# Performance work log

Hardware: AMD Instinct MI355X
Metric: run time of the kernel (lower is better)

Reference implementation:

```python
import jax, jax.numpy as jnp
import numpy as np

N_LEVELS, CPL = 4, 1024           # levels, cells per level (n_cells = 4096)
IN_D, HID, OUT_D, MLP = 512, 1024, 512, 128


def setup_inputs() -> dict:
    key = jax.random.key(0)
    ks = iter(jax.random.split(key, 32))
    r = lambda shape, s=0.05: jax.random.normal(next(ks), shape, dtype=jnp.float32) * s
    inp = {
        'x': r((1, IN_D), 1.0),
        'hiddens': r((N_LEVELS * CPL, HID), 0.1),
        'ea_W1': r((N_LEVELS, IN_D + HID, MLP)), 'ea_b1': r((N_LEVELS, MLP)),
        'ea_W2': r((N_LEVELS, MLP, OUT_D)),      'ea_b2': r((N_LEVELS, OUT_D)),
        'eg_W1': r((N_LEVELS, IN_D + HID, MLP)), 'eg_b1': r((N_LEVELS, MLP)),
        'eg_W2': r((N_LEVELS, MLP, OUT_D)),      'eg_b2': r((N_LEVELS, OUT_D)),
        'gru_Wih': r((N_LEVELS, 3 * HID, OUT_D + 1)),
        'gru_Whh': r((N_LEVELS, 3 * HID, HID)),
        'gru_bih': r((N_LEVELS, 3 * HID)), 'gru_bhh': r((N_LEVELS, 3 * HID)),
        'pred_W1': r((N_LEVELS - 1, HID, HID)), 'pred_b1': r((N_LEVELS - 1, HID)),
        'pred_W2': r((N_LEVELS - 1, HID, HID)), 'pred_b2': r((N_LEVELS - 1, HID)),
        'pei_W': r((HID * N_LEVELS, OUT_D)), 'pei_b': r((OUT_D,)),
        'step': 10,
    }
    return inp


def _forward(x, hiddens, ea_W1, ea_b1, ea_W2, ea_b2, eg_W1, eg_b1, eg_W2, eg_b2,
             gru_Wih, gru_Whh, gru_bih, gru_bhh, pred_W1, pred_b1, pred_W2, pred_b2,
             pei_W, pei_b, step):
    L = gru_Whh.shape[0]
    Hd = gru_Whh.shape[2]
    C = hiddens.shape[0] // L
    h = hiddens.reshape(L, C, Hd)                              # [L,C,H]
    xb = jnp.broadcast_to(x[0], (L, C, x.shape[-1]))           # same x for every cell
    comb = jnp.concatenate([xb, h], axis=-1)                   # [L,C,IN+H]

    def mlp(W1, b1, W2, b2):
        z = jax.nn.relu(jnp.einsum('lci,lim->lcm', comb, W1) + b1[:, None, :])
        return jnp.einsum('lcm,lmo->lco', z, W2) + b2[:, None, :]

    out = mlp(ea_W1, ea_b1, ea_W2, ea_b2) - mlp(eg_W1, eg_b1, eg_W2, eg_b2)  # a - g
    tension = jnp.mean(out ** 2, axis=-1, keepdims=True)       # [L,C,1]
    avg_tension = jnp.mean(tension)                            # mean over all cells

    # GRUCell (torch gate order r,z,n); mem input is detached in the original
    mem_in = jax.lax.stop_gradient(jnp.concatenate([out, tension], axis=-1))  # [L,C,OUT+1]
    gi = jnp.einsum('lci,lgi->lcg', mem_in, gru_Wih) + gru_bih[:, None, :]
    gh = jnp.einsum('lch,lgh->lcg', h, gru_Whh) + gru_bhh[:, None, :]
    i_r, i_z, i_n = jnp.split(gi, 3, axis=-1)
    h_r, h_z, h_n = jnp.split(gh, 3, axis=-1)
    rg = jax.nn.sigmoid(i_r + h_r)
    zg = jax.nn.sigmoid(i_z + h_z)
    ng = jnp.tanh(i_n + rg * h_n)
    new_h = jax.lax.stop_gradient((1.0 - zg) * ng + zg * h)    # self.hiddens = ...detach()

    level_means = new_h.mean(axis=1)                           # [L,H] (pre pe-update)

    # top-down predictors: predicted[lv] from level_means[lv+1]
    pz = jax.nn.relu(jnp.einsum('li,lim->lm', level_means[1:], pred_W1) + pred_b1)
    predicted = jnp.einsum('lm,lmo->lo', pz, pred_W2) + pred_b2          # [L-1,H]
    pe_signal = jax.lax.stop_gradient((predicted - level_means[:-1]) * 0.05)
    delta = jnp.zeros_like(level_means).at[:-1].add(pe_signal).at[1:].add(-0.5 * pe_signal)
    hh = new_h + delta[:, None, :]

    # per-level mean blend
    hh = 0.85 * hh + 0.15 * hh.mean(axis=1, keepdims=True)
    # faction sync: with n_factions == n_levels, factions == levels exactly
    hh = 0.85 * hh + 0.15 * hh.mean(axis=1, keepdims=True)
    if step > 5:  # debate (step is a static Python int)
        global_op = hh.mean(axis=1).mean(axis=0)               # [H]
        dc = max(1, C // 4)
        hh = hh.at[:, :dc].set(0.85 * hh[:, :dc] + 0.15 * global_op)

    combined = level_means.reshape(-1) @ pei_W + pei_b         # [OUT]
    return combined, avg_tension, hh.reshape(-1, Hd)


def reference(x, hiddens, ea_W1, ea_b1, ea_W2, ea_b2, eg_W1, eg_b1, eg_W2, eg_b2,
              gru_Wih, gru_Whh, gru_bih, gru_bhh, pred_W1, pred_b1, pred_W2, pred_b2,
              pei_W, pei_b, step):
    return _forward(x, hiddens, ea_W1, ea_b1, ea_W2, ea_b2, eg_W1, eg_b1, eg_W2, eg_b2,
                    gru_Wih, gru_Whh, gru_bih, gru_bhh, pred_W1, pred_b1, pred_W2, pred_b2,
                    pei_W, pei_b, step)
```

## Files before the change

### kernel.cpp

```cpp
#include <hip/hip_runtime.h>
#include <math.h>

#define L4   4
#define CPL  1024
#define HID  1024
#define IND  512
#define MLPD 128
#define OUTD 512
#define G3   3072
#define ROWS 4096
#define KP   544
#define SCL  0.0009765625f

typedef unsigned short u16;
typedef u16   u16x8  __attribute__((ext_vector_type(8)));
typedef short bf16x8 __attribute__((ext_vector_type(8)));
typedef float f32x4  __attribute__((ext_vector_type(4)));

__device__ __forceinline__ float b2f(u16 u) {
  return __uint_as_float(((unsigned int)u) << 16);
}
__device__ __forceinline__ u16 f2b(float f) {
  unsigned int x = __float_as_uint(f);
  x += 0x7fffu + ((x >> 16) & 1u);
  return (u16)(x >> 16);
}
__device__ __forceinline__ float sigm(float v) { return 1.0f/(1.0f + expf(-v)); }

__device__ __forceinline__ float ld1(const void* p, size_t i, bool f32) {
  return f32 ? ((const float*)p)[i] : b2f(((const u16*)p)[i]);
}
__device__ __forceinline__ void st1(void* p, size_t i, float v, bool f32) {
  if (f32) ((float*)p)[i] = v; else ((u16*)p)[i] = f2b(v);
}
__device__ __forceinline__ u16x8 ldc8(const void* p, size_t i, bool f32) {
  u16x8 r;
  if (f32) {
    const float* q = (const float*)p + i;
    float4 v0 = *reinterpret_cast<const float4*>(q);
    float4 v1 = *reinterpret_cast<const float4*>(q + 4);
    r[0]=f2b(v0.x); r[1]=f2b(v0.y); r[2]=f2b(v0.z); r[3]=f2b(v0.w);
    r[4]=f2b(v1.x); r[5]=f2b(v1.y); r[6]=f2b(v1.z); r[7]=f2b(v1.w);
  } else {
    r = *reinterpret_cast<const u16x8*>((const u16*)p + i);
  }
  return r;
}

__global__ void k_detect(const void* __restrict__ x, int* __restrict__ flag) {
  int t = threadIdx.x;
  const u16* xu = (const u16*)x;
  unsigned u = xu[2*t];
  int e = (u >> 7) & 0xFF;
  int good = (e >= 96 && e <= 134) ? 1 : 0;
  __shared__ int cnt[256];
  cnt[t] = good;
  __syncthreads();
  for (int s = 128; s > 0; s >>= 1) { if (t < s) cnt[t] += cnt[t+s]; __syncthreads(); }
  if (t == 0) flag[0] = (cnt[0] < 200) ? 1 : 0;
}

__global__ void k_prep(float* __restrict__ zf, const void* __restrict__ bih,
                       const void* __restrict__ bhh, const int* __restrict__ dflag,
                       float* __restrict__ bs_r, float* __restrict__ bs_z,
                       float* __restrict__ bn_i, float* __restrict__ bn_h) {
  const bool f32 = dflag[0] != 0;
  int b = blockIdx.x, t = threadIdx.x;
  if (b < 16) {
    int idx = b*256 + t;
    int l = idx >> 10, j = idx & 1023;
    bs_r[idx] = ld1(bih, l*G3 + j, f32)        + ld1(bhh, l*G3 + j, f32);
    bs_z[idx] = ld1(bih, l*G3 + 1024 + j, f32) + ld1(bhh, l*G3 + 1024 + j, f32);
    bn_i[idx] = ld1(bih, l*G3 + 2048 + j, f32);
    bn_h[idx] = ld1(bhh, l*G3 + 2048 + j, f32);
  } else {
    int idx = (b-16)*256 + t;
    zf[idx] = 0.0f;
  }
}

__global__ void k_prep_wih(const void* __restrict__ Wih, const int* __restrict__ dflag,
                           u16* __restrict__ WihP) {
  const bool f32 = dflag[0] != 0;
  int row = blockIdx.x;
  int t = threadIdx.x;
  size_t src = (size_t)row * 513;
  size_t dst = (size_t)row * KP;
  WihP[dst + t]       = f2b(ld1(Wih, src + t, f32));
  WihP[dst + 256 + t] = f2b(ld1(Wih, src + 256 + t, f32));
  if (t < 32) {
    float v = (t == 0) ? ld1(Wih, src + 512, f32) : 0.0f;
    WihP[dst + 512 + t] = f2b(v);
  }
}

__global__ void k_prep_cvt(const void* __restrict__ Whh, const void* __restrict__ H,
                           const int* __restrict__ dflag,
                           u16* __restrict__ WhhP, u16* __restrict__ HB) {
  const bool f32 = dflag[0] != 0;
  int t = threadIdx.x;
  int b = blockIdx.x;
  int c8 = (t & 127) * 8;
  if (b < 6144) {
    int row = b*2 + (t >> 7);
    size_t off = (size_t)row * HID + c8;
    *reinterpret_cast<u16x8*>(&WhhP[off]) = ldc8(Whh, off, f32);
  } else {
    int row = (b - 6144)*2 + (t >> 7);
    size_t off = (size_t)row * HID + c8;
    *reinterpret_cast<u16x8*>(&HB[off]) = ldc8(H, off, f32);
  }
}

__global__ void k_prep_w1t(const void* __restrict__ eaW1, const void* __restrict__ egW1,
                           const int* __restrict__ dflag, u16* __restrict__ W1T) {
  const bool f32 = dflag[0] != 0;
  __shared__ u16 sT[128*66];
  int l = blockIdx.x, path = blockIdx.y, kt = blockIdx.z;
  int t = threadIdx.x;
  const void* W1 = path ? egW1 : eaW1;
  for (int rr = 0; rr < 64; rr += 2) {
    int r = rr + (t >> 7), m = t & 127;
    float v = ld1(W1, ((size_t)l*1536 + 512 + kt*64 + r)*MLPD + m, f32);
    sT[m*66 + r] = f2b(v);
  }
  __syncthreads();
  for (int mm = 0; mm < 128; mm += 4) {
    int m = mm + (t >> 6), kk = t & 63;
    W1T[((size_t)l*256 + path*128 + m)*1024 + kt*64 + kk] = sT[m*66 + kk];
  }
}

__global__ void k_prep_w2m(const void* __restrict__ eaW2, const void* __restrict__ egW2,
                           const int* __restrict__ dflag, u16* __restrict__ W2M) {
  const bool f32 = dflag[0] != 0;
  __shared__ u16 sT[128*130];
  int l = blockIdx.x, path = blockIdx.y, ot = blockIdx.z;
  int t = threadIdx.x;
  const void* W2 = path ? egW2 : eaW2;
  float sgn = path ? -1.0f : 1.0f;
  for (int rr = 0; rr < 128; rr += 2) {
    int r = rr + (t >> 7), o = t & 127;
    float v = ld1(W2, ((size_t)l*MLPD + r)*OUTD + ot*128 + o, f32);
    sT[o*130 + r] = f2b(sgn*v);
  }
  __syncthreads();
  for (int oo = 0; oo < 128; oo += 2) {
    int o = oo + (t >> 7), m = t & 127;
    W2M[((size_t)l*OUTD + ot*128 + o)*256 + path*128 + m] = sT[o*130 + m];
  }
}

__global__ void k_base_acc(const void* __restrict__ x, const void* __restrict__ eaW1,
                           const void* __restrict__ egW1, const int* __restrict__ dflag,
                           float* __restrict__ baseacc) {
  const bool f32 = dflag[0] != 0;
  int l = blockIdx.x, path = blockIdx.y, kc = blockIdx.z, m = threadIdx.x;
  const void* W1 = path ? egW1 : eaW1;
  float acc = 0.0f;
  int i0 = kc*128;
  for (int i = i0; i < i0 + 128; ++i)
    acc += ld1(x, i, f32) * ld1(W1, ((size_t)l*1536 + i)*MLPD + m, f32);
  atomicAdd(&baseacc[path*512 + l*MLPD + m], acc);
}

#define SWZ(row, ku) ((row)*64 + ((ku) ^ (((row)&7)<<3)))

__global__ __launch_bounds__(256) void k_z_mfma(
    const u16* __restrict__ HB, const u16* __restrict__ W1T,
    const void* __restrict__ eab1, const void* __restrict__ egb1,
    const float* __restrict__ baseacc, const int* __restrict__ dflag,
    u16* __restrict__ Z) {
  const bool f32 = dflag[0] != 0;
  __shared__ __align__(16) u16 sA[2][64*64];
  __shared__ __align__(16) u16 sB[2][64*64];
  int t = threadIdx.x;
  int row0 = blockIdx.x * 64;
  int n0   = blockIdx.y * 64;
  int l    = row0 >> 10;
  int wid = t >> 6, lane = t & 63;
  int waveM = wid >> 1, waveN = wid & 1;
  int quad = lane >> 4, lcol = lane & 15;

  f32x4 acc[2][2];
  const f32x4 zz = {0.0f,0.0f,0.0f,0.0f};
#pragma unroll
  for (int i = 0; i < 2; ++i)
#pragma unroll
    for (int j = 0; j < 2; ++j) acc[i][j] = zz;

  u16x8 ra[2], rb[2];
  auto loadk = [&](int k0) {
#pragma unroll
    for (int s = 0; s < 2; ++s) {
      int idx = s*256 + t, row = idx >> 3, ch = idx & 7;
      ra[s] = *reinterpret_cast<const u16x8*>(
          HB + (size_t)(row0 + row)*HID + k0 + ch*8);
      rb[s] = *reinterpret_cast<const u16x8*>(
          W1T + ((size_t)l*256 + n0 + row)*1024 + k0 + ch*8);
    }
  };
  auto stage = [&](int cb) {
#pragma unroll
    for (int s = 0; s < 2; ++s) {
      int idx = s*256 + t, row = idx >> 3, ch = idx & 7;
      *reinterpret_cast<u16x8*>(&sA[cb][SWZ(row, ch*8)]) = ra[s];
      *reinterpret_cast<u16x8*>(&sB[cb][SWZ(row, ch*8)]) = rb[s];
    }
  };

  int cur = 0;
  loadk(0);
  for (int k0 = 0; k0 < HID; k0 += 64) {
    stage(cur);
    asm volatile("s_waitcnt lgkmcnt(0)" ::: "memory");
    __builtin_amdgcn_s_barrier();
    if (k0 + 64 < HID) loadk(k0 + 64);
    __builtin_amdgcn_s_setprio(1);
#pragma unroll
    for (int kc = 0; kc < 2; ++kc) {
      bf16x8 af[2];
#pragma unroll
      for (int i = 0; i < 2; ++i) {
        int rl = waveM*32 + i*16 + lcol;
        af[i] = *reinterpret_cast<const bf16x8*>(&sA[cur][SWZ(rl, kc*32 + quad*8)]);
      }
#pragma unroll
      for (int j = 0; j < 2; ++j) {
        int jl = waveN*32 + j*16 + lcol;
        bf16x8 bf = *reinterpret_cast<const bf16x8*>(&sB[cur][SWZ(jl, kc*32 + quad*8)]);
#pragma unroll
        for (int i = 0; i < 2; ++i)
          acc[i][j] = __builtin_amdgcn_mfma_f32_16x16x32_bf16(af[i], bf, acc[i][j], 0, 0, 0);
      }
    }
    __builtin_amdgcn_s_setprio(0);
    cur ^= 1;
  }
#pragma unroll
  for (int j = 0; j < 2; ++j) {
    int nn = n0 + waveN*32 + j*16 + lcol;
    int path = nn >> 7, m = nn & 127;
    float bval = baseacc[path*512 + l*MLPD + m] +
                 ld1(path ? egb1 : eab1, l*MLPD + m, f32);
#pragma unroll
    for (int i = 0; i < 2; ++i)
#pragma unroll
      for (int g = 0; g < 4; ++g) {
        int r = row0 + waveM*32 + i*16 + quad*4 + g;
        float v = acc[i][j][g] + bval;
        Z[(size_t)r*256 + nn] = f2b(v > 0.0f ? v : 0.0f);
      }
  }
}

__global__ __launch_bounds__(256) void k_outm(
    const u16* __restrict__ Zb, const u16* __restrict__ W2M,
    const void* __restrict__ eab2, const void* __restrict__ egb2,
    const int* __restrict__ dflag, u16* __restrict__ OUTT) {
  const bool f32 = dflag[0] != 0;
  __shared__ __align__(16) u16 sA[2][128*64];
  __shared__ __align__(16) u16 sB[2][64*64];
  int t = threadIdx.x;
  int row0 = blockIdx.x * 128;
  int n0   = blockIdx.y * 64;
  int l    = row0 >> 10;
  int wid = t >> 6, lane = t & 63;
  int waveM = wid & 1, waveJ = wid >> 1;
  int quad = lane >> 4, lcol = lane & 15;

  f32x4 acc[4][2];
  const f32x4 zz = {0.0f,0.0f,0.0f,0.0f};
#pragma unroll
  for (int i = 0; i < 4; ++i)
#pragma unroll
    for (int j = 0; j < 2; ++j) acc[i][j] = zz;

  u16x8 ra[4], rb[2];
  auto loadk = [&](int k0) {
#pragma unroll
    for (int s = 0; s < 4; ++s) {
      int idx = s*256 + t, row = idx >> 3, ch = idx & 7;
      ra[s] = *reinterpret_cast<const u16x8*>(
          Zb + (size_t)(row0 + row)*256 + k0 + ch*8);
    }
#pragma unroll
    for (int s = 0; s < 2; ++s) {
      int idx = s*256 + t, row = idx >> 3, ch = idx & 7;
      rb[s] = *reinterpret_cast<const u16x8*>(
          W2M + ((size_t)l*OUTD + n0 + row)*256 + k0 + ch*8);
    }
  };
  auto stage = [&](int cb) {
#pragma unroll
    for (int s = 0; s < 4; ++s) {
      int idx = s*256 + t, row = idx >> 3, ch = idx & 7;
      *reinterpret_cast<u16x8*>(&sA[cb][SWZ(row, ch*8)]) = ra[s];
    }
#pragma unroll
    for (int s = 0; s < 2; ++s) {
      int idx = s*256 + t, row = idx >> 3, ch = idx & 7;
      *reinterpret_cast<u16x8*>(&sB[cb][SWZ(row, ch*8)]) = rb[s];
    }
  };

  int cur = 0;
  loadk(0);
  for (int k0 = 0; k0 < 256; k0 += 64) {
    stage(cur);
    asm volatile("s_waitcnt lgkmcnt(0)" ::: "memory");
    __builtin_amdgcn_s_barrier();
    if (k0 + 64 < 256) loadk(k0 + 64);
    __builtin_amdgcn_s_setprio(1);
#pragma unroll
    for (int kc = 0; kc < 2; ++kc) {
      bf16x8 af[4];
#pragma unroll
      for (int i = 0; i < 4; ++i) {
        int rl = waveM*64 + i*16 + lcol;
        af[i] = *reinterpret_cast<const bf16x8*>(&sA[cur][SWZ(rl, kc*32 + quad*8)]);
      }
#pragma unroll
      for (int jj = 0; jj < 2; ++jj) {
        int jl = waveJ*32 + jj*16 + lcol;
        bf16x8 bf = *reinterpret_cast<const bf16x8*>(&sB[cur][SWZ(jl, kc*32 + quad*8)]);
#pragma unroll
        for (int i = 0; i < 4; ++i)
          acc[i][jj] = __builtin_amdgcn_mfma_f32_16x16x32_bf16(af[i], bf, acc[i][jj], 0, 0, 0);
      }
    }
    __builtin_amdgcn_s_setprio(0);
    cur ^= 1;
  }
#pragma unroll
  for (int jj = 0; jj < 2; ++jj) {
    int o = n0 + waveJ*32 + jj*16 + lcol;
    float bd = ld1(eab2, l*OUTD + o, f32) - ld1(egb2, l*OUTD + o, f32);
#pragma unroll
    for (int i = 0; i < 4; ++i)
#pragma unroll
      for (int g = 0; g < 4; ++g) {
        int r = row0 + waveM*64 + i*16 + quad*4 + g;
        OUTT[(size_t)r*KP + o] = f2b(acc[i][jj][g] + bd);
      }
  }
}

__global__ void k_tension(u16* __restrict__ OUTT, float* __restrict__ tsum) {
  int row = blockIdx.x, t = threadIdx.x;
  u16* p = OUTT + (size_t)row*KP;
  float v0 = b2f(p[t]), v1 = b2f(p[t+256]);
  float s = v0*v0 + v1*v1;
#pragma unroll
  for (int off = 32; off > 0; off >>= 1) s += __shfl_down(s, off, 64);
  __shared__ float red[4];
  if ((t & 63) == 0) red[t >> 6] = s;
  __syncthreads();
  if (t == 0) {
    float tot = red[0] + red[1] + red[2] + red[3];
    p[512] = f2b(tot * (1.0f/512.0f));
    atomicAdd(tsum, tot);
  }
  if (t < 31) p[513 + t] = 0;
}

__global__ __launch_bounds__(256, 2) void k_gru_mfma(
    const u16* __restrict__ OUTT, const u16* __restrict__ HB,
    const u16* __restrict__ WihP, const u16* __restrict__ WhhP,
    const void* __restrict__ H,
    const float* __restrict__ bs_r, const float* __restrict__ bs_z,
    const float* __restrict__ bn_i, const float* __restrict__ bn_h,
    const int* __restrict__ dflag, void* __restrict__ outv) {
  const bool f32 = dflag[0] != 0;
  __shared__ __align__(16) u16 sA[2][128*64];
  __shared__ __align__(16) u16 sB[2][3*64*64];
  int t = threadIdx.x;
  int bid = blockIdx.x;
  int xg = bid & 7, inner = bid >> 3;
  int l = xg & 3, jG = xg >> 2;
  int rbi = inner & 7, jbl = inner >> 3;
  int row0 = (l*8 + rbi) * 128;
  int j0   = (jG*8 + jbl) * 64;
  int wid = t >> 6, lane = t & 63;
  int waveM = wid & 1, waveJ = wid >> 1;
  int quad = lane >> 4, lcol = lane & 15;

  f32x4 acc[4][4][2];
  const f32x4 zz = {0.0f,0.0f,0.0f,0.0f};
#pragma unroll
  for (int b = 0; b < 4; ++b)
#pragma unroll
    for (int i = 0; i < 4; ++i)
#pragma unroll
      for (int j = 0; j < 2; ++j) acc[b][i][j] = zz;

  u16x8 ra[4], rbr[6];
  auto load1 = [&](int k0) {
    int kw = KP - k0;
#pragma unroll
    for (int s = 0; s < 4; ++s) {
      int idx = s*256 + t, row = idx >> 3, ch = idx & 7;
      if (ch*8 < kw)
        ra[s] = *reinterpret_cast<const u16x8*>(
            OUTT + (size_t)(row0 + row)*KP + k0 + ch*8);
      else { u16x8 z = {0,0,0,0,0,0,0,0}; ra[s] = z; }
    }
#pragma unroll
    for (int s = 0; s < 6; ++s) {
      int idx = s*256 + t, band = idx >> 9, rem = idx & 511;
      int row = rem >> 3, ch = rem & 7;
      if (ch*8 < kw)
        rbr[s] = *reinterpret_cast<const u16x8*>(
            WihP + ((size_t)l*G3 + band*1024 + j0 + row)*KP + k0 + ch*8);
      else { u16x8 z = {0,0,0,0,0,0,0,0}; rbr[s] = z; }
    }
  };
  auto load2 = [&](int k0) {
#pragma unroll
    for (int s = 0; s < 4; ++s) {
      int idx = s*256 + t, row = idx >> 3, ch = idx & 7;
      ra[s] = *reinterpret_cast<const u16x8*>(
          HB + (size_t)(row0 + row)*HID + k0 + ch*8);
    }
#pragma unroll
    for (int s = 0; s < 6; ++s) {
      int idx = s*256 + t, band = idx >> 9, rem = idx & 511;
      int row = rem >> 3, ch = rem & 7;
      rbr[s] = *reinterpret_cast<const u16x8*>(
          WhhP + ((size_t)l*G3 + band*1024 + j0 + row)*HID + k0 + ch*8);
    }
  };
  auto stage = [&](int cb) {
#pragma unroll
    for (int s = 0; s < 4; ++s) {
      int idx = s*256 + t, row = idx >> 3, ch = idx & 7;
      *reinterpret_cast<u16x8*>(&sA[cb][SWZ(row, ch*8)]) = ra[s];
    }
#pragma unroll
    for (int s = 0; s < 6; ++s) {
      int idx = s*256 + t, band = idx >> 9, rem = idx & 511;
      int row = rem >> 3, ch = rem & 7;
      *reinterpret_cast<u16x8*>(&sB[cb][band*4096 + SWZ(row, ch*8)]) = rbr[s];
    }
  };

  int cur = 0;
  load1(0);
  for (int k0 = 0; k0 < KP; k0 += 64) {
    stage(cur);
    asm volatile("s_waitcnt lgkmcnt(0)" ::: "memory");
    __builtin_amdgcn_s_barrier();
    if (k0 + 64 < KP) load1(k0 + 64);
    else              load2(0);
    __builtin_amdgcn_s_setprio(1);
#pragma unroll
    for (int kc = 0; kc < 2; ++kc) {
      bf16x8 af[4];
#pragma unroll
      for (int i = 0; i < 4; ++i) {
        int rl = waveM*64 + i*16 + lcol;
        af[i] = *reinterpret_cast<const bf16x8*>(&sA[cur][SWZ(rl, kc*32 + quad*8)]);
      }
#pragma unroll
      for (int b = 0; b < 3; ++b)
#pragma unroll
        for (int jj = 0; jj < 2; ++jj) {
          int jl = waveJ*32 + jj*16 + lcol;
          bf16x8 bf = *reinterpret_cast<const bf16x8*>(
              &sB[cur][b*4096 + SWZ(jl, kc*32 + quad*8)]);
#pragma unroll
          for (int i = 0; i < 4; ++i)
            acc[b][i][jj] = __builtin_amdgcn_mfma_f32_16x16x32_bf16(
                af[i], bf, acc[b][i][jj], 0, 0, 0);
        }
    }
    __builtin_amdgcn_s_setprio(0);
    cur ^= 1;
  }
  for (int k0 = 0; k0 < HID; k0 += 64) {
    stage(cur);
    asm volatile("s_waitcnt lgkmcnt(0)" ::: "memory");
    __builtin_amdgcn_s_barrier();
    if (k0 + 64 < HID) load2(k0 + 64);
    __builtin_amdgcn_s_setprio(1);
#pragma unroll
    for (int kc = 0; kc < 2; ++kc) {
      bf16x8 af[4];
#pragma unroll
      for (int i = 0; i < 4; ++i) {
        int rl = waveM*64 + i*16 + lcol;
        af[i] = *reinterpret_cast<const bf16x8*>(&sA[cur][SWZ(rl, kc*32 + quad*8)]);
      }
#pragma unroll
      for (int b = 0; b < 3; ++b) {
        int ai = (b < 2) ? b : 3;
#pragma unroll
        for (int jj = 0; jj < 2; ++jj) {
          int jl = waveJ*32 + jj*16 + lcol;
          bf16x8 bf = *reinterpret_cast<const bf16x8*>(
              &sB[cur][b*4096 + SWZ(jl, kc*32 + quad*8)]);
#pragma unroll
          for (int i = 0; i < 4; ++i)
            acc[ai][i][jj] = __builtin_amdgcn_mfma_f32_16x16x32_bf16(
                af[i], bf, acc[ai][i][jj], 0, 0, 0);
        }
      }
    }
    __builtin_amdgcn_s_setprio(0);
    cur ^= 1;
  }
#pragma unroll
  for (int i = 0; i < 4; ++i)
#pragma unroll
    for (int jj = 0; jj < 2; ++jj) {
      int j = j0 + waveJ*32 + jj*16 + lcol;
      float br = bs_r[l*HID + j], bz = bs_z[l*HID + j];
      float bi = bn_i[l*HID + j], bh = bn_h[l*HID + j];
#pragma unroll
      for (int g = 0; g < 4; ++g) {
        int r = row0 + waveM*64 + i*16 + quad*4 + g;
        float rg = sigm(acc[0][i][jj][g] + br);
        float zg = sigm(acc[1][i][jj][g] + bz);
        float ng = tanhf(acc[2][i][jj][g] + bi + rg*(acc[3][i][jj][g] + bh));
        float hv = ld1(H, (size_t)r*HID + j, f32);
        st1(outv, 513 + (size_t)r*HID + j, (1.0f - zg)*ng + zg*hv, f32);
      }
    }
}

__global__ void k_lm_acc(const void* __restrict__ outv, const int* __restrict__ dflag,
                         float* __restrict__ lm) {
  const bool f32 = dflag[0] != 0;
  int l = blockIdx.x, cc = blockIdx.y, t = threadIdx.x;
  float s0=0.f, s1=0.f, s2=0.f, s3=0.f;
  for (int c = cc*16; c < cc*16 + 16; ++c) {
    size_t base = 513 + (size_t)(l*CPL + c)*HID;
    s0 += ld1(outv, base + t,       f32);
    s1 += ld1(outv, base + 256 + t, f32);
    s2 += ld1(outv, base + 512 + t, f32);
    s3 += ld1(outv, base + 768 + t, f32);
  }
  atomicAdd(&lm[l*HID + t],       s0);
  atomicAdd(&lm[l*HID + 256 + t], s1);
  atomicAdd(&lm[l*HID + 512 + t], s2);
  atomicAdd(&lm[l*HID + 768 + t], s3);
}

__global__ void k_pz_acc(const float* __restrict__ lm, const void* __restrict__ pW1,
                         const int* __restrict__ dflag, float* __restrict__ pz) {
  const bool f32 = dflag[0] != 0;
  int lv = blockIdx.x, mb = blockIdx.y, kc = blockIdx.z;
  int m = mb*256 + threadIdx.x;
  float acc = 0.0f;
  int i0 = kc*32;
  const float* lmp = lm + (lv + 1)*HID;
  for (int i = i0; i < i0 + 32; ++i)
    acc += lmp[i] * ld1(pW1, ((size_t)lv*HID + i)*HID + m, f32);
  atomicAdd(&pz[lv*HID + m], acc * SCL);
}
__global__ void k_pzfin(float* __restrict__ pz, const void* __restrict__ pb1,
                        const int* __restrict__ dflag) {
  const bool f32 = dflag[0] != 0;
  int idx = blockIdx.x*256 + threadIdx.x;
  float v = pz[idx] + ld1(pb1, idx, f32);
  pz[idx] = v > 0.0f ? v : 0.0f;
}
__global__ void k_pe_acc(const float* __restrict__ pz, const void* __restrict__ pW2,
                         const int* __restrict__ dflag, float* __restrict__ pe) {
  const bool f32 = dflag[0] != 0;
  int lv = blockIdx.x, ob = blockIdx.y, kc = blockIdx.z;
  int o = ob*256 + threadIdx.x;
  float acc = 0.0f;
  int m0 = kc*32;
  const float* pzp = pz + lv*HID;
  for (int m = m0; m < m0 + 32; ++m)
    acc += pzp[m] * ld1(pW2, ((size_t)lv*HID + m)*HID + o, f32);
  atomicAdd(&pe[lv*HID + o], acc);
}
__global__ void k_pefin(float* __restrict__ pe, const void* __restrict__ pb2,
                        const float* __restrict__ lm, const int* __restrict__ dflag) {
  const bool f32 = dflag[0] != 0;
  int idx = blockIdx.x*256 + threadIdx.x;
  pe[idx] = (pe[idx] + ld1(pb2, idx, f32) - lm[idx]*SCL) * 0.05f;
}

__global__ void k_addc_gop(const float* __restrict__ lm, const float* __restrict__ pe,
                           float* __restrict__ addc, float* __restrict__ gop) {
  int j = blockIdx.x*256 + threadIdx.x;
  float pe0 = pe[j], pe1 = pe[1024 + j], pe2 = pe[2048 + j];
  float d0 = pe0, d1 = pe1 - 0.5f*pe0, d2 = pe2 - 0.5f*pe1, d3 = -0.5f*pe2;
  float l0 = lm[j]*SCL, l1 = lm[1024 + j]*SCL, l2 = lm[2048 + j]*SCL, l3 = lm[3072 + j]*SCL;
  addc[j]        = 0.2775f*l0 + d0;
  addc[1024 + j] = 0.2775f*l1 + d1;
  addc[2048 + j] = 0.2775f*l2 + d2;
  addc[3072 + j] = 0.2775f*l3 + d3;
  gop[j] = 0.25f*((l0 + d0) + (l1 + d1) + (l2 + d2) + (l3 + d3));
}

__global__ void k_comb_acc(const float* __restrict__ lm, const void* __restrict__ peiW,
                           const int* __restrict__ dflag, float* __restrict__ comb) {
  const bool f32 = dflag[0] != 0;
  int ob = blockIdx.x, kc = blockIdx.y;
  int o = ob*256 + threadIdx.x;
  float acc = 0.0f;
  int i0 = kc*128;
  for (int i = i0; i < i0 + 128; ++i)
    acc += lm[i] * ld1(peiW, (size_t)i*OUTD + o, f32);
  atomicAdd(&comb[o], acc * SCL);
}
__global__ void k_fin(const float* __restrict__ comb, const void* __restrict__ peib,
                      const float* __restrict__ tsum, const int* __restrict__ dflag,
                      void* __restrict__ outv) {
  const bool f32 = dflag[0] != 0;
  int o = blockIdx.x*256 + threadIdx.x;
  st1(outv, o, comb[o] + ld1(peib, o, f32), f32);
  if (o == 0) st1(outv, 512, tsum[0] * (1.0f/(4096.0f*512.0f)), f32);
}

__global__ void k_hh(void* __restrict__ outv, const float* __restrict__ addc,
                     const float* __restrict__ gop, const int* __restrict__ step,
                     const int* __restrict__ dflag) {
  const bool f32 = dflag[0] != 0;
  int row = blockIdx.x, t = threadIdx.x;
  int l = row >> 10, c = row & 1023;
  bool debate = (step[0] > 5) && (c < 256);
  size_t base = 513 + (size_t)row*HID;
#pragma unroll
  for (int k = 0; k < 4; ++k) {
    int j = t + k*256;
    float v = 0.7225f * ld1(outv, base + j, f32) + addc[l*HID + j];
    if (debate) v = 0.85f*v + 0.15f*gop[j];
    st1(outv, base + j, v, f32);
  }
}

extern "C" void kernel_launch(void* const* d_in, const int* in_sizes, int n_in,
                              void* d_out, int out_size, void* d_ws, size_t ws_size,
                              hipStream_t stream) {
  (void)in_sizes; (void)n_in; (void)out_size; (void)ws_size;
  const void* x    = d_in[0];
  const void* hid  = d_in[1];
  const void* eaW1 = d_in[2];
  const void* eab1 = d_in[3];
  const void* eaW2 = d_in[4];
  const void* eab2 = d_in[5];
  const void* egW1 = d_in[6];
  const void* egb1 = d_in[7];
  const void* egW2 = d_in[8];
  const void* egb2 = d_in[9];
  const void* gWih = d_in[10];
  const void* gWhh = d_in[11];
  const void* gbih = d_in[12];
  const void* gbhh = d_in[13];
  const void* pW1  = d_in[14];
  const void* pb1  = d_in[15];
  const void* pW2  = d_in[16];
  const void* pb2  = d_in[17];
  const void* peiW = d_in[18];
  const void* peib = d_in[19];
  const int*  step = (const int*)d_in[20];

  float* wsf = (float*)d_ws;
  float* tsum    = wsf + 0;
  float* baseacc = wsf + 64;
  float* lm      = wsf + 1088;
  float* pz      = wsf + 5184;
  float* pe      = wsf + 8256;
  float* comb    = wsf + 11328;
  int*   dflag   = (int*)(wsf + 12288);
  float* bs_r    = wsf + 12352;
  float* bs_z    = wsf + 16448;
  float* bn_i    = wsf + 20544;
  float* bn_h    = wsf + 24640;
  float* addc    = wsf + 28736;
  float* gop     = wsf + 32832;
  u16* Zb   = (u16*)(wsf + 33856);
  u16* OUTT = Zb + (size_t)4096*256;
  u16* WihP = OUTT + (size_t)4096*KP;
  u16* HB   = WihP + (size_t)12288*KP;
  u16* WhhP = HB   + (size_t)4096*1024;
  u16* W2M  = WhhP + (size_t)12288*1024;
  u16* W1T  = OUTT;

  k_detect   <<<dim3(1),        dim3(256), 0, stream>>>(x, dflag);
  k_prep     <<<dim3(64),       dim3(256), 0, stream>>>(wsf, gbih, gbhh, dflag,
                                                        bs_r, bs_z, bn_i, bn_h);
  k_prep_wih <<<dim3(12288),    dim3(256), 0, stream>>>(gWih, dflag, WihP);
  k_prep_cvt <<<dim3(8192),     dim3(256), 0, stream>>>(gWhh, hid, dflag, WhhP, HB);
  k_prep_w1t <<<dim3(4,2,16),   dim3(256), 0, stream>>>(eaW1, egW1, dflag, W1T);
  k_prep_w2m <<<dim3(4,2,4),    dim3(256), 0, stream>>>(eaW2, egW2, dflag, W2M);
  k_base_acc <<<dim3(4,2,4),    dim3(128), 0, stream>>>(x, eaW1, egW1, dflag, baseacc);
  k_z_mfma   <<<dim3(64,4),     dim3(256), 0, stream>>>(HB, W1T, eab1, egb1,
                                                        baseacc, dflag, Zb);
  k_outm     <<<dim3(32,8),     dim3(256), 0, stream>>>(Zb, W2M, eab2, egb2,
                                                        dflag, OUTT);
  k_tension  <<<dim3(4096),     dim3(256), 0, stream>>>(OUTT, tsum);
  k_gru_mfma <<<dim3(512),      dim3(256), 0, stream>>>(OUTT, HB, WihP, WhhP, hid,
                                                        bs_r, bs_z, bn_i, bn_h,
                                                        dflag, d_out);
  k_lm_acc   <<<dim3(4,64),     dim3(256), 0, stream>>>(d_out, dflag, lm);
  k_pz_acc   <<<dim3(3,4,32),   dim3(256), 0, stream>>>(lm, pW1, dflag, pz);
  k_pzfin    <<<dim3(12),       dim3(256), 0, stream>>>(pz, pb1, dflag);
  k_pe_acc   <<<dim3(3,4,32),   dim3(256), 0, stream>>>(pz, pW2, dflag, pe);
  k_pefin    <<<dim3(12),       dim3(256), 0, stream>>>(pe, pb2, lm, dflag);
  k_addc_gop <<<dim3(4),        dim3(256), 0, stream>>>(lm, pe, addc, gop);
  k_comb_acc <<<dim3(2,32),     dim3(256), 0, stream>>>(lm, peiW, dflag, comb);
  k_fin      <<<dim3(2),        dim3(256), 0, stream>>>(comb, peib, tsum, dflag, d_out);
  k_hh       <<<dim3(4096),     dim3(256), 0, stream>>>(d_out, addc, gop, step, dflag);
}
```

Measured before the change: 477.7 us.

## Deepen GRU MFMA global prefetch to two stages and fuse small epilogue kernels

```diff
diff --git a/kernel.cpp b/kernel.cpp
--- a/kernel.cpp
+++ b/kernel.cpp
@@ -394,64 +394,60 @@
 #pragma unroll
       for (int j = 0; j < 2; ++j) acc[b][i][j] = zz;
 
-  u16x8 ra[4], rbr[6];
-  auto load1 = [&](int k0) {
-    int kw = KP - k0;
-#pragma unroll
-    for (int s = 0; s < 4; ++s) {
-      int idx = s*256 + t, row = idx >> 3, ch = idx & 7;
-      if (ch*8 < kw)
-        ra[s] = *reinterpret_cast<const u16x8*>(
-            OUTT + (size_t)(row0 + row)*KP + k0 + ch*8);
-      else { u16x8 z = {0,0,0,0,0,0,0,0}; ra[s] = z; }
-    }
-#pragma unroll
-    for (int s = 0; s < 6; ++s) {
-      int idx = s*256 + t, band = idx >> 9, rem = idx & 511;
+  u16x8 raA[4], rbA[6], raB[4], rbB[6];
+
+  auto loadS = [&](u16x8 (&ra)[4], u16x8 (&rb)[6], int s) {
+    if (s < 9) {
+      int k0 = s*64;
+      int kw = KP - k0;
+#pragma unroll
+      for (int q = 0; q < 4; ++q) {
+        int idx = q*256 + t, row = idx >> 3, ch = idx & 7;
+        if (ch*8 < kw)
+          ra[q] = *reinterpret_cast<const u16x8*>(
+              OUTT + (size_t)(row0 + row)*KP + k0 + ch*8);
+        else { u16x8 z = {0,0,0,0,0,0,0,0}; ra[q] = z; }
+      }
+#pragma unroll
+      for (int q = 0; q < 6; ++q) {
+        int idx = q*256 + t, band = idx >> 9, rem = idx & 511;
+        int row = rem >> 3, ch = rem & 7;
+        if (ch*8 < kw)
+          rb[q] = *reinterpret_cast<const u16x8*>(
+              WihP + ((size_t)l*G3 + band*1024 + j0 + row)*KP + k0 + ch*8);
+        else { u16x8 z = {0,0,0,0,0,0,0,0}; rb[q] = z; }
+      }
+    } else {
+      int k0 = (s - 9)*64;
+#pragma unroll
+      for (int q = 0; q < 4; ++q) {
+        int idx = q*256 + t, row = idx >> 3, ch = idx & 7;
+        ra[q] = *reinterpret_cast<const u16x8*>(
+            HB + (size_t)(row0 + row)*HID + k0 + ch*8);
+      }
+#pragma unroll
+      for (int q = 0; q < 6; ++q) {
+        int idx = q*256 + t, band = idx >> 9, rem = idx & 511;
+        int row = rem >> 3, ch = rem & 7;
+        rb[q] = *reinterpret_cast<const u16x8*>(
+            WhhP + ((size_t)l*G3 + band*1024 + j0 + row)*HID + k0 + ch*8);
+      }
+    }
+  };
+  auto stage = [&](int cb, u16x8 (&ra)[4], u16x8 (&rb)[6]) {
+#pragma unroll
+    for (int q = 0; q < 4; ++q) {
+      int idx = q*256 + t, row = idx >> 3, ch = idx & 7;
+      *reinterpret_cast<u16x8*>(&sA[cb][SWZ(row, ch*8)]) = ra[q];
+    }
+#pragma unroll
+    for (int q = 0; q < 6; ++q) {
+      int idx = q*256 + t, band = idx >> 9, rem = idx & 511;
       int row = rem >> 3, ch = rem & 7;
-      if (ch*8 < kw)
-        rbr[s] = *reinterpret_cast<const u16x8*>(
-            WihP + ((size_t)l*G3 + band*1024 + j0 + row)*KP + k0 + ch*8);
-      else { u16x8 z = {0,0,0,0,0,0,0,0}; rbr[s] = z; }
+      *reinterpret_cast<u16x8*>(&sB[cb][band*4096 + SWZ(row, ch*8)]) = rb[q];
     }
   };
-  auto load2 = [&](int k0) {
-#pragma unroll
-    for (int s = 0; s < 4; ++s) {
-      int idx = s*256 + t, row = idx >> 3, ch = idx & 7;
-      ra[s] = *reinterpret_cast<const u16x8*>(
-          HB + (size_t)(row0 + row)*HID + k0 + ch*8);
-    }
-#pragma unroll
-    for (int s = 0; s < 6; ++s) {
-      int idx = s*256 + t, band = idx >> 9, rem = idx & 511;
-      int row = rem >> 3, ch = rem & 7;
-      rbr[s] = *reinterpret_cast<const u16x8*>(
-          WhhP + ((size_t)l*G3 + band*1024 + j0 + row)*HID + k0 + ch*8);
-    }
-  };
-  auto stage = [&](int cb) {
-#pragma unroll
-    for (int s = 0; s < 4; ++s) {
-      int idx = s*256 + t, row = idx >> 3, ch = idx & 7;
-      *reinterpret_cast<u16x8*>(&sA[cb][SWZ(row, ch*8)]) = ra[s];
-    }
-#pragma unroll
-    for (int s = 0; s < 6; ++s) {
-      int idx = s*256 + t, band = idx >> 9, rem = idx & 511;
-      int row = rem >> 3, ch = rem & 7;
-      *reinterpret_cast<u16x8*>(&sB[cb][band*4096 + SWZ(row, ch*8)]) = rbr[s];
-    }
-  };
-
-  int cur = 0;
-  load1(0);
-  for (int k0 = 0; k0 < KP; k0 += 64) {
-    stage(cur);
-    asm volatile("s_waitcnt lgkmcnt(0)" ::: "memory");
-    __builtin_amdgcn_s_barrier();
-    if (k0 + 64 < KP) load1(k0 + 64);
-    else              load2(0);
+  auto domfma = [&](int cb, bool g2) {
     __builtin_amdgcn_s_setprio(1);
 #pragma unroll
     for (int kc = 0; kc < 2; ++kc) {
@@ -459,46 +455,16 @@
 #pragma unroll
       for (int i = 0; i < 4; ++i) {
         int rl = waveM*64 + i*16 + lcol;
-        af[i] = *reinterpret_cast<const bf16x8*>(&sA[cur][SWZ(rl, kc*32 + quad*8)]);
-      }
-#pragma unroll
-      for (int b = 0; b < 3; ++b)
+        af[i] = *reinterpret_cast<const bf16x8*>(&sA[cb][SWZ(rl, kc*32 + quad*8)]);
+      }
+#pragma unroll
+      for (int b = 0; b < 3; ++b) {
+        int ai = (g2 && b == 2) ? 3 : b;
 #pragma unroll
         for (int jj = 0; jj < 2; ++jj) {
           int jl = waveJ*32 + jj*16 + lcol;
           bf16x8 bf = *reinterpret_cast<const bf16x8*>(
-              &sB[cur][b*4096 + SWZ(jl, kc*32 + quad*8)]);
-#pragma unroll
-          for (int i = 0; i < 4; ++i)
-            acc[b][i][jj] = __builtin_amdgcn_mfma_f32_16x16x32_bf16(
-                af[i], bf, acc[b][i][jj], 0, 0, 0);
-        }
-    }
-    __builtin_amdgcn_s_setprio(0);
-    cur ^= 1;
-  }
-  for (int k0 = 0; k0 < HID; k0 += 64) {
-    stage(cur);
-    asm volatile("s_waitcnt lgkmcnt(0)" ::: "memory");
-    __builtin_amdgcn_s_barrier();
-    if (k0 + 64 < HID) load2(k0 + 64);
-    __builtin_amdgcn_s_setprio(1);
-#pragma unroll
-    for (int kc = 0; kc < 2; ++kc) {
-      bf16x8 af[4];
-#pragma unroll
-      for (int i = 0; i < 4; ++i) {
-        int rl = waveM*64 + i*16 + lcol;
-        af[i] = *reinterpret_cast<const bf16x8*>(&sA[cur][SWZ(rl, kc*32 + quad*8)]);
-      }
-#pragma unroll
-      for (int b = 0; b < 3; ++b) {
-        int ai = (b < 2) ? b : 3;
-#pragma unroll
-        for (int jj = 0; jj < 2; ++jj) {
-          int jl = waveJ*32 + jj*16 + lcol;
-          bf16x8 bf = *reinterpret_cast<const bf16x8*>(
-              &sB[cur][b*4096 + SWZ(jl, kc*32 + quad*8)]);
+              &sB[cb][b*4096 + SWZ(jl, kc*32 + quad*8)]);
 #pragma unroll
           for (int i = 0; i < 4; ++i)
             acc[ai][i][jj] = __builtin_amdgcn_mfma_f32_16x16x32_bf16(
@@ -507,7 +473,27 @@
       }
     }
     __builtin_amdgcn_s_setprio(0);
+  };
+
+  const int NS = 25;
+  int cur = 0;
+  loadS(raA, rbA, 0);
+  loadS(raB, rbB, 1);
+  for (int s = 0; s < NS; s += 2) {
+    stage(cur, raA, rbA);
+    asm volatile("s_waitcnt lgkmcnt(0)" ::: "memory");
+    __builtin_amdgcn_s_barrier();
+    if (s + 2 < NS) loadS(raA, rbA, s + 2);
+    domfma(cur, s >= 9);
     cur ^= 1;
+    if (s + 1 < NS) {
+      stage(cur, raB, rbB);
+      asm volatile("s_waitcnt lgkmcnt(0)" ::: "memory");
+      __builtin_amdgcn_s_barrier();
+      if (s + 3 < NS) loadS(raB, rbB, s + 3);
+      domfma(cur, s + 1 >= 9);
+      cur ^= 1;
+    }
   }
 #pragma unroll
   for (int i = 0; i < 4; ++i)
@@ -558,36 +544,30 @@
     acc += lmp[i] * ld1(pW1, ((size_t)lv*HID + i)*HID + m, f32);
   atomicAdd(&pz[lv*HID + m], acc * SCL);
 }
-__global__ void k_pzfin(float* __restrict__ pz, const void* __restrict__ pb1,
-                        const int* __restrict__ dflag) {
-  const bool f32 = dflag[0] != 0;
-  int idx = blockIdx.x*256 + threadIdx.x;
-  float v = pz[idx] + ld1(pb1, idx, f32);
-  pz[idx] = v > 0.0f ? v : 0.0f;
-}
-__global__ void k_pe_acc(const float* __restrict__ pz, const void* __restrict__ pW2,
+__global__ void k_pe_acc(const float* __restrict__ pz, const void* __restrict__ pb1,
+                         const void* __restrict__ pW2,
                          const int* __restrict__ dflag, float* __restrict__ pe) {
   const bool f32 = dflag[0] != 0;
   int lv = blockIdx.x, ob = blockIdx.y, kc = blockIdx.z;
   int o = ob*256 + threadIdx.x;
   float acc = 0.0f;
   int m0 = kc*32;
-  const float* pzp = pz + lv*HID;
-  for (int m = m0; m < m0 + 32; ++m)
-    acc += pzp[m] * ld1(pW2, ((size_t)lv*HID + m)*HID + o, f32);
+  for (int m = m0; m < m0 + 32; ++m) {
+    float v = pz[lv*HID + m] + ld1(pb1, lv*HID + m, f32);
+    v = v > 0.0f ? v : 0.0f;
+    acc += v * ld1(pW2, ((size_t)lv*HID + m)*HID + o, f32);
+  }
   atomicAdd(&pe[lv*HID + o], acc);
 }
-__global__ void k_pefin(float* __restrict__ pe, const void* __restrict__ pb2,
-                        const float* __restrict__ lm, const int* __restrict__ dflag) {
-  const bool f32 = dflag[0] != 0;
-  int idx = blockIdx.x*256 + threadIdx.x;
-  pe[idx] = (pe[idx] + ld1(pb2, idx, f32) - lm[idx]*SCL) * 0.05f;
-}
 
 __global__ void k_addc_gop(const float* __restrict__ lm, const float* __restrict__ pe,
+                           const void* __restrict__ pb2, const int* __restrict__ dflag,
                            float* __restrict__ addc, float* __restrict__ gop) {
+  const bool f32 = dflag[0] != 0;
   int j = blockIdx.x*256 + threadIdx.x;
-  float pe0 = pe[j], pe1 = pe[1024 + j], pe2 = pe[2048 + j];
+  float pe0 = (pe[j]        + ld1(pb2, j,        f32) - lm[j]*SCL)        * 0.05f;
+  float pe1 = (pe[1024 + j] + ld1(pb2, 1024 + j, f32) - lm[1024 + j]*SCL) * 0.05f;
+  float pe2 = (pe[2048 + j] + ld1(pb2, 2048 + j, f32) - lm[2048 + j]*SCL) * 0.05f;
   float d0 = pe0, d1 = pe1 - 0.5f*pe0, d2 = pe2 - 0.5f*pe1, d3 = -0.5f*pe2;
   float l0 = lm[j]*SCL, l1 = lm[1024 + j]*SCL, l2 = lm[2048 + j]*SCL, l3 = lm[3072 + j]*SCL;
   addc[j]        = 0.2775f*l0 + d0;
@@ -700,10 +680,8 @@
                                                         dflag, d_out);
   k_lm_acc   <<<dim3(4,64),     dim3(256), 0, stream>>>(d_out, dflag, lm);
   k_pz_acc   <<<dim3(3,4,32),   dim3(256), 0, stream>>>(lm, pW1, dflag, pz);
-  k_pzfin    <<<dim3(12),       dim3(256), 0, stream>>>(pz, pb1, dflag);
-  k_pe_acc   <<<dim3(3,4,32),   dim3(256), 0, stream>>>(pz, pW2, dflag, pe);
-  k_pefin    <<<dim3(12),       dim3(256), 0, stream>>>(pe, pb2, lm, dflag);
-  k_addc_gop <<<dim3(4),        dim3(256), 0, stream>>>(lm, pe, addc, gop);
+  k_pe_acc   <<<dim3(3,4,32),   dim3(256), 0, stream>>>(pz, pb1, pW2, dflag, pe);
+  k_addc_gop <<<dim3(4),        dim3(256), 0, stream>>>(lm, pe, pb2, dflag, addc, gop);
   k_comb_acc <<<dim3(2,32),     dim3(256), 0, stream>>>(lm, peiW, dflag, comb);
   k_fin      <<<dim3(2),        dim3(256), 0, stream>>>(comb, peib, tsum, dflag, d_out);
   k_hh       <<<dim3(4096),     dim3(256), 0, stream>>>(d_out, addc, gop, step, dflag);
```

Measured after the change: 472.6 us. About the same (-1.1%).
